# Kernel tuning notes

Hardware: AMD Instinct MI355X
Metric: run time of the kernel (lower is better)

Reference implementation:

```python
import jax, jax.numpy as jnp
import numpy as np

# Dimensions
B = 256        # number of graphs
NPG = 128      # nodes per graph (max_nodes; uniform -> to_dense_batch == reshape)
H = 8          # num_heads
DH = 32        # head_dim
HID = H * DH   # hidden_dim = 256
E = 524288     # n_edges
NGT = 20       # num_gate_types
EF = 8         # edge_feat_dim


def setup_inputs() -> dict:
    key = jax.random.key(0)
    ks = jax.random.split(key, 20)
    n_nodes = B * NPG
    x = jax.random.normal(ks[0], (n_nodes, HID), jnp.float32)
    # edges stay within the source node's graph
    src = jax.random.randint(ks[1], (E,), 0, n_nodes, dtype=jnp.int32)
    dst = (src // NPG) * NPG + jax.random.randint(ks[2], (E,), 0, NPG, dtype=jnp.int32)
    edge_index = jnp.stack([src, dst])  # [2, E]
    edge_attr = jax.random.normal(ks[3], (E, EF), jnp.float32)
    edge_gate_type = jax.random.randint(ks[4], (E,), 0, NGT, dtype=jnp.int32)
    batch = (jnp.arange(n_nodes) // NPG).astype(jnp.int32)

    s = 1.0 / np.sqrt(HID)
    def lin(k, din, dout, scale):
        kw, kb = jax.random.split(k)
        return (jax.random.uniform(kw, (din, dout), jnp.float32, -scale, scale),
                jax.random.uniform(kb, (dout,), jnp.float32, -scale, scale))
    Wq, bq = lin(ks[5], HID, HID, s)
    Wk, bk = lin(ks[6], HID, HID, s)
    Wv, bv = lin(ks[7], HID, HID, s)
    Wo, bo = lin(ks[8], HID, HID, s)
    gate_table = jax.random.normal(ks[9], (NGT, H), jnp.float32)
    We, be = lin(ks[10], EF, H, 1.0 / np.sqrt(EF))
    return {"x": x, "edge_attr": edge_attr, "Wq": Wq, "bq": bq, "Wk": Wk, "bk": bk,
            "Wv": Wv, "bv": bv, "Wo": Wo, "bo": bo, "gate_table": gate_table,
            "We": We, "be": be, "edge_index": edge_index,
            "edge_gate_type": edge_gate_type, "batch": batch}


def _edge_bias(edge_index, edge_attr, edge_gate_type, batch, gate_table, We, be):
    src, dst = edge_index[0], edge_index[1]
    eb = batch[src]                       # edge -> graph id
    src_l = src - eb * NPG                # local node index within graph
    dst_l = dst - eb * NPG
    total = gate_table[edge_gate_type] + edge_attr @ We + be   # [E, H]
    bias = jnp.zeros((B, H, NPG, NPG), edge_attr.dtype)
    bias = bias.at[eb, :, src_l, dst_l].add(total)             # forward direction
    rev = jnp.where((src_l != dst_l)[:, None], total, 0.0)     # skip self-loops
    bias = bias.at[eb, :, dst_l, src_l].add(rev)               # reverse direction
    return bias


def reference(x, edge_attr, Wq, bq, Wk, bk, Wv, bv, Wo, bo, gate_table, We, be,
              edge_index, edge_gate_type, batch):
    scale = 1.0 / np.sqrt(DH)
    xd = x.reshape(B, NPG, HID)  # uniform graph sizes -> to_dense_batch is a reshape
    Q = (xd @ Wq + bq).reshape(B, NPG, H, DH).transpose(0, 2, 1, 3)  # [B,H,N,D]
    K = (xd @ Wk + bk).reshape(B, NPG, H, DH).transpose(0, 2, 1, 3)
    V = (xd @ Wv + bv).reshape(B, NPG, H, DH).transpose(0, 2, 1, 3)
    scores = jnp.einsum('bhqd,bhkd->bhqk', Q, K) * scale
    scores = scores + _edge_bias(edge_index, edge_attr, edge_gate_type, batch,
                                 gate_table, We, be)
    attn = jax.nn.softmax(scores, axis=-1)  # node_mask all-True (uniform sizes)
    out = jnp.einsum('bhqk,bhkd->bhqd', attn, V)
    out = out.transpose(0, 2, 1, 3).reshape(B * NPG, HID)
    return out @ Wo + bo
```

## Files before the change

### kernel.cpp

```cpp
#include <hip/hip_runtime.h>
#include <hip/hip_fp16.h>

typedef unsigned short u16;
typedef unsigned int u32;
typedef __attribute__((ext_vector_type(8))) short short8;
typedef __attribute__((ext_vector_type(4))) float f32x4;

#define MFMA16(a, b, c) __builtin_amdgcn_mfma_f32_16x16x32_bf16((a), (b), (c), 0, 0, 0)

#define ESTRIDE 2304

#define FIXSCALE 16777216.0f
#define FIXINV   5.9604644775390625e-8f

__device__ __forceinline__ float b2f(u16 u) {
  union { float f; unsigned int i; } v;
  v.i = ((unsigned int)u) << 16;
  return v.f;
}
__device__ __forceinline__ u16 f2b(float f) {
  union { float f; unsigned int i; } v;
  v.f = f;
  unsigned int x = v.i;
  return (u16)((x + 0x7FFFu + ((x >> 16) & 1u)) >> 16);
}
__device__ __forceinline__ u16 f2h_bits(float f) {
  __half h = __float2half(f);
  u16 b;
  __builtin_memcpy(&b, &h, 2);
  return b;
}
__device__ __forceinline__ float h2f_bits(u16 b) {
  __half h;
  __builtin_memcpy(&h, &b, 2);
  return __half2float(h);
}

__device__ __forceinline__ void gload_lds16(const u16* g, u16* l) {
  __builtin_amdgcn_global_load_lds(
      (const __attribute__((address_space(1))) void*)g,
      (__attribute__((address_space(3))) void*)l, 16, 0, 0);
}

__global__ __launch_bounds__(256) void cvt_wtrans_kernel(
    const float* __restrict__ x, u16* __restrict__ xb,
    const float* __restrict__ W0, const float* __restrict__ W1,
    const float* __restrict__ W2, const float* __restrict__ W3,
    u16* __restrict__ T0, u16* __restrict__ T1,
    u16* __restrict__ T2, u16* __restrict__ T3,
    u32* __restrict__ gfill) {
  int bx = blockIdx.x;
  if (bx < 4096) {
    size_t i = ((size_t)bx * 256 + threadIdx.x) * 8;
    const float4* p = (const float4*)(x + i);
    float4 v0 = p[0], v1 = p[1];
    float vf[8] = {v0.x, v0.y, v0.z, v0.w, v1.x, v1.y, v1.z, v1.w};
    short8 s;
#pragma unroll
    for (int j = 0; j < 8; ++j) s[j] = (short)f2b(vf[j]);
    *(short8*)(xb + i) = s;
  } else if (bx < 4224) {
    int r = bx - 4096;
    const float* W; u16* T;
    switch (r >> 5) {
      case 0: W = W0; T = T0; break;
      case 1: W = W1; T = T1; break;
      case 2: W = W2; T = T2; break;
      default: W = W3; T = T3; break;
    }
    int n = threadIdx.x;
    int k0 = (r & 31) * 8;
    short8 s;
#pragma unroll
    for (int j = 0; j < 8; ++j) s[j] = (short)f2b(W[(size_t)(k0 + j) * 256 + n]);
    *(short8*)(T + (size_t)n * 256 + k0) = s;
  } else {
    int idx = (bx - 4224) * 256 + threadIdx.x;
    gfill[idx] = 0;
  }
}

__global__ __launch_bounds__(256) void edge_build_kernel(
    const int* __restrict__ ei, const float* __restrict__ ea,
    const int* __restrict__ egt, const float* __restrict__ gate_table,
    const float* __restrict__ We, const float* __restrict__ be,
    u32* __restrict__ gfill, u16* __restrict__ etot16,
    u32* __restrict__ epos, int E) {
  __shared__ u32 hist[256];
  __shared__ u32 cursor[256];
  const int tid = threadIdx.x;
  hist[tid] = 0;
  __syncthreads();
  const int base_e = blockIdx.x * 2048;
  int gcache[8];
#pragma unroll
  for (int i = 0; i < 8; ++i) {
    int e = base_e + i * 256 + tid;
    int g = (e < E) ? (ei[e] >> 7) : -1;
    gcache[i] = g;
    if (g >= 0) atomicAdd(&hist[(u32)g], 1u);
  }
  __syncthreads();
  {
    u32 c = hist[tid];
    u32 r = c ? atomicAdd(&gfill[tid * 16], c) : 0u;
    cursor[tid] = (u32)tid * ESTRIDE + r;
  }
  __syncthreads();
#pragma unroll
  for (int i = 0; i < 8; ++i) {
    int g = gcache[i];
    if (g < 0) continue;
    int e = base_e + i * 256 + tid;
    int src = ei[e], dst = ei[E + e];
    int sl = src & 127, dl = dst & 127;
    int gt = egt[e];
    const float4* eap = (const float4*)(ea + (size_t)e * 8);
    float4 e0 = eap[0], e1 = eap[1];
    float eaf[8] = {e0.x, e0.y, e0.z, e0.w, e1.x, e1.y, e1.z, e1.w};
    short8 sv;
#pragma unroll
    for (int h = 0; h < 8; ++h) {
      float s = gate_table[gt * 8 + h] + be[h];
#pragma unroll
      for (int f = 0; f < 8; ++f) s += eaf[f] * We[f * 8 + h];
      sv[h] = (short)f2h_bits(s);
    }
    u32 pos = atomicAdd(&cursor[(u32)g], 1u);
    epos[pos] = (u32)sl | ((u32)dl << 16);
    *(short8*)(etot16 + (size_t)pos * 8) = sv;
  }
}

template <int NMAT, typename COUT>
__global__ __launch_bounds__(256) void gemm_tiled_kernel(
    const u16* __restrict__ A,
    const u16* __restrict__ T0, const u16* __restrict__ T1,
    const u16* __restrict__ T2,
    const float* __restrict__ b0, const float* __restrict__ b1,
    const float* __restrict__ b2,
    float s0, float s1, float s2,
    COUT* __restrict__ C0, COUT* __restrict__ C1, COUT* __restrict__ C2) {
  __shared__ __align__(16) u16 lA[128 * 64];
  __shared__ __align__(16) u16 lB[128 * 64];

  const int tid = threadIdx.x;
  const int bm = blockIdx.x;
  const int bn = blockIdx.y;
  const int m  = (NMAT == 1) ? 0 : (bn >> 1);
  const int ch = (NMAT == 1) ? bn : (bn & 1);

  const u16* Ts[3] = {T0, T1, T2};
  const float* bs[3] = {b0, b1, b2};
  const float scs[3] = {s0, s1, s2};
  COUT* Cs[3] = {C0, C1, C2};

  const u16* Abase = A + (size_t)(bm * 128) * 256;
  const u16* Bbase = Ts[m] + (size_t)(ch * 128) * 256;

  int srow[4];
  int selem[4];
#pragma unroll
  for (int i = 0; i < 4; ++i) {
    int c = i * 256 + tid;
    int row = c >> 3;
    int q = (c & 7) * 16;
    srow[i] = row;
    selem[i] = (q ^ ((row & 7) << 4)) >> 1;
  }

  const int wid = tid >> 6, lane = tid & 63;
  const int wm = wid >> 1, wn = wid & 1;
  const int quad = lane >> 4, l16 = lane & 15;
  const int swz = (l16 & 7) << 4;

  f32x4 acc[4][4] = {};

#pragma unroll
  for (int kt = 0; kt < 4; ++kt) {
    const int k0 = kt * 64;
    __syncthreads();
#pragma unroll
    for (int i = 0; i < 4; ++i) {
      gload_lds16(Abase + (size_t)srow[i] * 256 + k0 + selem[i],
                  lA + (size_t)(i * 256 + tid) * 8);
      gload_lds16(Bbase + (size_t)srow[i] * 256 + k0 + selem[i],
                  lB + (size_t)(i * 256 + tid) * 8);
    }
    __syncthreads();

#pragma unroll
    for (int ks = 0; ks < 2; ++ks) {
      const int kb = (ks * 64 + quad * 16) ^ swz;
      short8 af[4], bf[4];
#pragma unroll
      for (int i = 0; i < 4; ++i) {
        int arow = wm * 64 + i * 16 + l16;
        af[i] = *(const short8*)((const char*)lA + arow * 128 + kb);
        int brow = wn * 64 + i * 16 + l16;
        bf[i] = *(const short8*)((const char*)lB + brow * 128 + kb);
      }
#pragma unroll
      for (int i = 0; i < 4; ++i)
#pragma unroll
        for (int j = 0; j < 4; ++j)
          acc[i][j] = MFMA16(af[i], bf[j], acc[i][j]);
    }
  }

  const float* bias = bs[m];
  const float sc = scs[m];
  COUT* C = Cs[m];
#pragma unroll
  for (int j = 0; j < 4; ++j) {
    int col = ch * 128 + wn * 64 + j * 16 + l16;
    float bv = bias[col];
#pragma unroll
    for (int i = 0; i < 4; ++i) {
      int row0 = bm * 128 + wm * 64 + i * 16 + quad * 4;
#pragma unroll
      for (int r = 0; r < 4; ++r) {
        float o = (acc[i][j][r] + bv) * sc;
        if constexpr (sizeof(COUT) == 4)
          C[(size_t)(row0 + r) * 256 + col] = o;
        else
          C[(size_t)(row0 + r) * 256 + col] = f2b(o);
      }
    }
  }
}

__global__ __launch_bounds__(512) void attn_kernel(
    const u16* __restrict__ Q, const u16* __restrict__ K,
    const u16* __restrict__ V, const u32* __restrict__ epos,
    const u16* __restrict__ etot16, const u32* __restrict__ gfill,
    u16* __restrict__ O) {
  constexpr int LV = 144, LP = 136, LS = 132;
  __shared__ __align__(16) char smem[67584];
  int*   Si  = (int*)smem;
  u32*   Su  = (u32*)smem;
  u16*   Pb  = (u16*)smem;
  u16*   Vt  = (u16*)(smem + 34816);
  float* inv = (float*)(smem + 44032);

  const int tid = threadIdx.x;
  const int h = blockIdx.x, b = blockIdx.y;
  const int wid = tid >> 6, lane = tid & 63;
  const int quad = lane >> 4, l16 = lane & 15;

  const u32 cnt = gfill[b * 16];
  u32 pd[5]; u16 tb[5];
  {
    const u32* ep = epos + (size_t)b * ESTRIDE;
    const u16* ets = etot16 + ((size_t)b * ESTRIDE) * 8 + h;
#pragma unroll
    for (int i = 0; i < 4; ++i) pd[i] = ep[tid + i * 512];
#pragma unroll
    for (int i = 0; i < 4; ++i) tb[i] = ets[(size_t)(tid + i * 512) * 8];
    if (tid < 256) { pd[4] = ep[2048 + tid]; tb[4] = ets[(size_t)(2048 + tid) * 8]; }
  }

  const int vr = tid >> 2, vs = (tid & 3) * 8;
  short8 vreg = *(const short8*)(V + (size_t)(b * 128 + vr) * 256 + h * 32 + vs);

  {
    short8 aq = *(const short8*)(
        Q + (size_t)(b * 128 + wid * 16 + l16) * 256 + h * 32 + quad * 8);
#pragma unroll
    for (int j = 0; j < 8; ++j) {
      short8 bk = *(const short8*)(
          K + (size_t)(b * 128 + j * 16 + l16) * 256 + h * 32 + quad * 8);
      f32x4 z = {0.f, 0.f, 0.f, 0.f};
      f32x4 sv = MFMA16(aq, bk, z);
      const int cswz = (j >> 1) << 3;
#pragma unroll
      for (int r = 0; r < 4; ++r)
        Si[(wid * 16 + quad * 4 + r) * LS + ((j * 16 + l16) ^ cswz)] =
            __float2int_rn(sv[r] * FIXSCALE);
    }
  }
  __syncthreads();

#pragma unroll
  for (int i = 0; i < 5; ++i) {
    u32 slot = (i < 4) ? (u32)(tid + i * 512) : (u32)(2048 + tid);
    bool live = (i < 4 || tid < 256) && (slot < cnt);
    if (live) {
      int sl = pd[i] & 0xffff, dl = pd[i] >> 16;
      u32 ti = (u32)__float2int_rn(h2f_bits(tb[i]) * FIXSCALE);
      int dls = dl ^ ((dl & 0x60) >> 2);
      int sls = sl ^ ((sl & 0x60) >> 2);
      atomicAdd(&Su[sl * LS + dls], ti);
      if (sl != dl) atomicAdd(&Su[dl * LS + sls], ti);
    }
  }
  __syncthreads();

  {
    int row = tid >> 2, t4 = tid & 3, c0 = t4 * 32;
    const int* srow = &Si[row * LS];
    float sv[32];
#pragma unroll
    for (int k = 0; k < 8; ++k) {
      int4 v = *(const int4*)(srow + ((c0 + k * 4) ^ (t4 << 3)));
      sv[k * 4 + 0] = (float)v.x * FIXINV;
      sv[k * 4 + 1] = (float)v.y * FIXINV;
      sv[k * 4 + 2] = (float)v.z * FIXINV;
      sv[k * 4 + 3] = (float)v.w * FIXINV;
    }
    float m = -1e30f;
#pragma unroll
    for (int c = 0; c < 32; ++c) m = fmaxf(m, sv[c]);
    m = fmaxf(m, __shfl_xor(m, 1, 64));
    m = fmaxf(m, __shfl_xor(m, 2, 64));
    float sum = 0.f;
    short8 prow[4];
#pragma unroll
    for (int c = 0; c < 32; ++c) {
      float p = __expf(sv[c] - m);
      sum += p;
      prow[c >> 3][c & 7] = (short)f2b(p);
    }
    sum += __shfl_xor(sum, 1, 64);
    sum += __shfl_xor(sum, 2, 64);
    __syncthreads();
#pragma unroll
    for (int k = 0; k < 4; ++k)
      *(short8*)&Pb[row * LP + c0 + k * 8] = prow[k];
#pragma unroll
    for (int j = 0; j < 8; ++j)
      Vt[(vs + j) * LV + vr] = (u16)vreg[j];
    if (t4 == 0) inv[row] = 1.f / sum;
  }
  __syncthreads();

  f32x4 oacc[2] = {};
#pragma unroll
  for (int ks = 0; ks < 4; ++ks) {
    short8 ap = *(short8*)&Pb[(wid * 16 + l16) * LP + ks * 32 + quad * 8];
#pragma unroll
    for (int j = 0; j < 2; ++j) {
      short8 bv = *(short8*)&Vt[(j * 16 + l16) * LV + ks * 32 + quad * 8];
      oacc[j] = MFMA16(ap, bv, oacc[j]);
    }
  }
#pragma unroll
  for (int j = 0; j < 2; ++j)
#pragma unroll
    for (int r = 0; r < 4; ++r) {
      int qr = wid * 16 + quad * 4 + r;
      float iv = inv[qr];
      O[(size_t)(b * 128 + qr) * 256 + h * 32 + j * 16 + l16] =
          f2b(oacc[j][r] * iv);
    }
}


extern "C" void kernel_launch(void* const* d_in, const int* in_sizes, int n_in,
                              void* d_out, int out_size, void* d_ws, size_t ws_size,
                              hipStream_t stream) {
  const float* x    = (const float*)d_in[0];
  const float* ea   = (const float*)d_in[1];
  const float* Wq   = (const float*)d_in[2];
  const float* bq   = (const float*)d_in[3];
  const float* Wk   = (const float*)d_in[4];
  const float* bk   = (const float*)d_in[5];
  const float* Wv   = (const float*)d_in[6];
  const float* bv   = (const float*)d_in[7];
  const float* Wo   = (const float*)d_in[8];
  const float* bo   = (const float*)d_in[9];
  const float* gate = (const float*)d_in[10];
  const float* We   = (const float*)d_in[11];
  const float* be   = (const float*)d_in[12];
  const int*   ei   = (const int*)d_in[13];
  const int*   egt  = (const int*)d_in[14];
  const int    E    = in_sizes[14];

  const size_t matBytes = (size_t)32768 * 256 * 2;
  const size_t slots = (size_t)256 * ESTRIDE;

  char* ws = (char*)d_ws;
  u16* Qm = (u16*)ws;
  u16* Km = (u16*)(ws + matBytes);
  u16* Vm = (u16*)(ws + 2 * matBytes);
  u16* Om = (u16*)(ws + 3 * matBytes);
  u16* xb = Om;
  u16*   etA  = (u16*)(ws + 4 * matBytes);
  u32*   epos = (u32*)(etA + slots * 8);
  u32*   gfill = (u32*)((char*)epos + slots * 4);
  u16*   Wtq = (u16*)((char*)gfill + 4096 * 4);
  u16*   Wtk = Wtq + 65536;
  u16*   Wtv = Wtk + 65536;
  u16*   Wto = Wtv + 65536;

  cvt_wtrans_kernel<<<dim3(4240), dim3(256), 0, stream>>>(
      x, xb, Wq, Wk, Wv, Wo, Wtq, Wtk, Wtv, Wto, gfill);

  edge_build_kernel<<<dim3((E + 2047) / 2048), dim3(256), 0, stream>>>(
      ei, ea, egt, gate, We, be, gfill, etA, epos, E);

  const float qscale = 0.17677669529663687f;
  gemm_tiled_kernel<3, u16><<<dim3(256, 6), dim3(256), 0, stream>>>(
      xb, Wtq, Wtk, Wtv, bq, bk, bv, qscale, 1.f, 1.f, Qm, Km, Vm);

  attn_kernel<<<dim3(8, 256), dim3(512), 0, stream>>>(
      Qm, Km, Vm, epos, etA, gfill, Om);

  gemm_tiled_kernel<1, float><<<dim3(256, 2), dim3(256), 0, stream>>>(
      Om, Wto, nullptr, nullptr, bo, nullptr, nullptr, 1.f, 1.f, 1.f,
      (float*)d_out, nullptr, nullptr);
}
```

Before: 221.3 us.

## Split attention blocks by query half to halve LDS and raise occupancy

The attention kernel now runs one 256-thread block per (graph, head, query-half) instead of one 512-thread block per (graph, head), covering 64 query rows and cutting shared memory to about 34KB so more blocks fit per CU. Each block still reads every edge of its graph and keeps only edges whose source or destination row falls in its half, so edge loads are duplicated across the two halves. The grid is also reordered so the graph index is the fast dimension.

```diff
diff --git a/kernel.cpp b/kernel.cpp
--- a/kernel.cpp
+++ b/kernel.cpp
@@ -230,42 +230,50 @@
   }
 }
 
-__global__ __launch_bounds__(512) void attn_kernel(
+__global__ __launch_bounds__(256, 4) void attn_kernel(
     const u16* __restrict__ Q, const u16* __restrict__ K,
     const u16* __restrict__ V, const u32* __restrict__ epos,
     const u16* __restrict__ etot16, const u32* __restrict__ gfill,
     u16* __restrict__ O) {
   constexpr int LV = 144, LP = 136, LS = 132;
-  __shared__ __align__(16) char smem[67584];
+  constexpr int NE = ESTRIDE / 256;
+  __shared__ __align__(16) char smem[34048];
   int*   Si  = (int*)smem;
   u32*   Su  = (u32*)smem;
   u16*   Pb  = (u16*)smem;
-  u16*   Vt  = (u16*)(smem + 34816);
-  float* inv = (float*)(smem + 44032);
+  u16*   Vt  = (u16*)(smem + 17408);
+  float* inv = (float*)(smem + 33792);
 
   const int tid = threadIdx.x;
-  const int h = blockIdx.x, b = blockIdx.y;
+  const int b = blockIdx.x;
+  const int h = blockIdx.y >> 1;
+  const int qh = blockIdx.y & 1;
+  const int q0 = qh * 64;
   const int wid = tid >> 6, lane = tid & 63;
   const int quad = lane >> 4, l16 = lane & 15;
 
   const u32 cnt = gfill[b * 16];
-  u32 pd[5]; u16 tb[5];
+  u32 pd[NE]; u16 tb[NE];
   {
     const u32* ep = epos + (size_t)b * ESTRIDE;
     const u16* ets = etot16 + ((size_t)b * ESTRIDE) * 8 + h;
 #pragma unroll
-    for (int i = 0; i < 4; ++i) pd[i] = ep[tid + i * 512];
-#pragma unroll
-    for (int i = 0; i < 4; ++i) tb[i] = ets[(size_t)(tid + i * 512) * 8];
-    if (tid < 256) { pd[4] = ep[2048 + tid]; tb[4] = ets[(size_t)(2048 + tid) * 8]; }
-  }
-
-  const int vr = tid >> 2, vs = (tid & 3) * 8;
-  short8 vreg = *(const short8*)(V + (size_t)(b * 128 + vr) * 256 + h * 32 + vs);
+    for (int i = 0; i < NE; ++i) pd[i] = ep[tid + i * 256];
+#pragma unroll
+    for (int i = 0; i < NE; ++i) tb[i] = ets[(size_t)(tid + i * 256) * 8];
+  }
+
+  const int vr = tid >> 1, vs = (tid & 1) * 16;
+  short8 vreg0, vreg1;
+  {
+    const u16* p = V + (size_t)(b * 128 + vr) * 256 + h * 32 + vs;
+    vreg0 = *(const short8*)p;
+    vreg1 = *(const short8*)(p + 8);
+  }
 
   {
     short8 aq = *(const short8*)(
-        Q + (size_t)(b * 128 + wid * 16 + l16) * 256 + h * 32 + quad * 8);
+        Q + (size_t)(b * 128 + q0 + wid * 16 + l16) * 256 + h * 32 + quad * 8);
 #pragma unroll
     for (int j = 0; j < 8; ++j) {
       short8 bk = *(const short8*)(
@@ -282,16 +290,18 @@
   __syncthreads();
 
 #pragma unroll
-  for (int i = 0; i < 5; ++i) {
-    u32 slot = (i < 4) ? (u32)(tid + i * 512) : (u32)(2048 + tid);
-    bool live = (i < 4 || tid < 256) && (slot < cnt);
-    if (live) {
+  for (int i = 0; i < NE; ++i) {
+    u32 slot = (u32)(tid + i * 256);
+    if (slot < cnt) {
       int sl = pd[i] & 0xffff, dl = pd[i] >> 16;
-      u32 ti = (u32)__float2int_rn(h2f_bits(tb[i]) * FIXSCALE);
-      int dls = dl ^ ((dl & 0x60) >> 2);
-      int sls = sl ^ ((sl & 0x60) >> 2);
-      atomicAdd(&Su[sl * LS + dls], ti);
-      if (sl != dl) atomicAdd(&Su[dl * LS + sls], ti);
+      int sr = sl - q0, dr = dl - q0;
+      if (((unsigned)sr < 64u) | ((unsigned)dr < 64u)) {
+        u32 ti = (u32)__float2int_rn(h2f_bits(tb[i]) * FIXSCALE);
+        int dls = dl ^ ((dl & 0x60) >> 2);
+        int sls = sl ^ ((sl & 0x60) >> 2);
+        if ((unsigned)sr < 64u) atomicAdd(&Su[sr * LS + dls], ti);
+        if (sl != dl && (unsigned)dr < 64u) atomicAdd(&Su[dr * LS + sls], ti);
+      }
     }
   }
   __syncthreads();
@@ -328,8 +338,10 @@
     for (int k = 0; k < 4; ++k)
       *(short8*)&Pb[row * LP + c0 + k * 8] = prow[k];
 #pragma unroll
-    for (int j = 0; j < 8; ++j)
-      Vt[(vs + j) * LV + vr] = (u16)vreg[j];
+    for (int j = 0; j < 8; ++j) {
+      Vt[(vs + j) * LV + vr] = (u16)vreg0[j];
+      Vt[(vs + 8 + j) * LV + vr] = (u16)vreg1[j];
+    }
     if (t4 == 0) inv[row] = 1.f / sum;
   }
   __syncthreads();
@@ -350,7 +362,7 @@
     for (int r = 0; r < 4; ++r) {
       int qr = wid * 16 + quad * 4 + r;
       float iv = inv[qr];
-      O[(size_t)(b * 128 + qr) * 256 + h * 32 + j * 16 + l16] =
+      O[(size_t)(b * 128 + q0 + qr) * 256 + h * 32 + j * 16 + l16] =
           f2b(oacc[j][r] * iv);
     }
 }
@@ -403,7 +415,7 @@
   gemm_tiled_kernel<3, u16><<<dim3(256, 6), dim3(256), 0, stream>>>(
       xb, Wtq, Wtk, Wtv, bq, bk, bv, qscale, 1.f, 1.f, Qm, Km, Vm);
 
-  attn_kernel<<<dim3(8, 256), dim3(512), 0, stream>>>(
+  attn_kernel<<<dim3(256, 16), dim3(256), 0, stream>>>(
       Qm, Km, Vm, epos, etA, gfill, Om);
 
   gemm_tiled_kernel<1, float><<<dim3(256, 2), dim3(256), 0, stream>>>(
```

Result: slower. 226.1 us (+2.2%).
